# Kernel tuning notes

Hardware: AMD Instinct MI355X
Metric: run time of the kernel (lower is better)

## Reference

```python
import jax, jax.numpy as jnp
import numpy as np

PADDING_IDX = 0


def setup_inputs() -> dict:
    key = jax.random.key(0)
    k1, k2 = jax.random.split(key)
    B, S, D = 64, 2048, 128
    V = 200000
    grad_output = jax.random.normal(k1, (B, S, D), dtype=jnp.float32)
    indices = jax.random.randint(k2, (B, S), 0, V, dtype=jnp.int64)
    return {"grad_output": grad_output, "indices": indices, "num_embeddings": V}


def reference(grad_output, indices, num_embeddings):
    D = grad_output.shape[-1]
    flat_idx = indices.reshape(-1)                      # [B*S]
    flat_grad = grad_output.reshape(-1, D)              # [B*S, D]
    # Zero out contributions from padding positions; padding row stays 0,
    # matching the original (it never accumulates into padding_idx).
    mask = (flat_idx != PADDING_IDX)[:, None]           # [B*S, 1]
    masked_grad = jnp.where(mask, flat_grad, jnp.zeros((), dtype=flat_grad.dtype))
    dense_grad = jax.ops.segment_sum(masked_grad, flat_idx,
                                     num_segments=num_embeddings)
    return dense_grad.astype(jnp.float32)
```

## Files before the change

### kernel.cpp

```cpp
#include <hip/hip_runtime.h>


#define EMB_D   128
#define PAD_IDX 0
#define MAXC    8
#define OVF_CAP 16384

typedef float fvec4 __attribute__((ext_vector_type(4)));

__global__ void __launch_bounds__(256)
prefetch_zero(const float4* __restrict__ grad, long g4n,
              uint4* __restrict__ zreg, long zn4,
              float* __restrict__ sink) {
    long tid    = (long)blockIdx.x * 256 + threadIdx.x;
    long stride = (long)gridDim.x * 256;
    uint4 z = make_uint4(0u, 0u, 0u, 0u);
    for (long i = tid; i < zn4; i += stride) zreg[i] = z;
    float acc = 0.f;
    for (long i = tid; i < g4n; i += stride) {
        float4 g = grad[i];
        acc += g.x + g.y + g.z + g.w;
    }
    if (acc == 1234567.891f) sink[0] = acc;
}

__global__ void __launch_bounds__(256)
scatter_slots(const int* __restrict__ idx, unsigned* __restrict__ counts,
              unsigned* __restrict__ slots, unsigned* __restrict__ ovfcnt,
              uint2* __restrict__ ovf, int n) {
    int i = blockIdx.x * blockDim.x + threadIdx.x;
    if (i >= n) return;
    int e = idx[i];
    if (e == PAD_IDX) return;
    unsigned p = atomicAdd(&counts[e], 1u);
    if (p < MAXC) {
        slots[(size_t)e * MAXC + p] = (unsigned)i;
    } else {
        unsigned q = atomicAdd(ovfcnt, 1u);
        if (q < OVF_CAP) ovf[q] = make_uint2((unsigned)e, (unsigned)i);
    }
}

__global__ void __launch_bounds__(256)
reduce_write(const float* __restrict__ grad, const unsigned* __restrict__ counts,
             const uint4* __restrict__ slots4, const unsigned* __restrict__ ovfcnt,
             const uint2* __restrict__ ovf, float* __restrict__ out, int V) {
    int wid  = (blockIdx.x * 256 + (int)threadIdx.x) >> 6;
    int half = (threadIdx.x >> 5) & 1;
    int lane = threadIdx.x & 31;
    const float4* __restrict__ g4 = (const float4*)grad;

    int base = wid * 8;
    if (base >= V) return;

    int      vr[4];
    unsigned cs[4];
    uint4    s0[4];
    #pragma unroll
    for (int p = 0; p < 4; ++p) {
        int v = base + 2 * p + half;
        int vc = v < V ? v : V - 1;
        vr[p] = v;
        cs[p] = counts[vc];
        s0[p] = slots4[(size_t)vc * 2];
    }

    unsigned ia[4][4];
    float    msk[4][3];
    #pragma unroll
    for (int p = 0; p < 4; ++p) {
        unsigned c = cs[p];
        if (vr[p] >= V || vr[p] == PAD_IDX) c = 0u;
        cs[p] = c;
        uint4 s = s0[p];
        unsigned i0 = (c > 0u) ? s.x : 0u;
        ia[p][0] = i0;
        ia[p][1] = (c > 1u) ? s.y : i0;
        ia[p][2] = (c > 2u) ? s.z : i0;
        ia[p][3] = (c > 3u) ? s.w : i0;
        msk[p][0] = (c > 1u) ? 1.f : 0.f;
        msk[p][1] = (c > 2u) ? 1.f : 0.f;
        msk[p][2] = (c > 3u) ? 1.f : 0.f;
    }
    float4 g[4][4];
    #pragma unroll
    for (int p = 0; p < 4; ++p)
        #pragma unroll
        for (int k = 0; k < 4; ++k)
            g[p][k] = g4[(size_t)ia[p][k] * 32 + lane];

    float4 acc[4];
    #pragma unroll
    for (int p = 0; p < 4; ++p) {
        float z  = (cs[p] > 0u) ? 1.f : 0.f;
        float m1 = msk[p][0], m2 = msk[p][1], m3 = msk[p][2];
        acc[p].x = z * g[p][0].x + m1 * g[p][1].x + m2 * g[p][2].x + m3 * g[p][3].x;
        acc[p].y = z * g[p][0].y + m1 * g[p][1].y + m2 * g[p][2].y + m3 * g[p][3].y;
        acc[p].z = z * g[p][0].z + m1 * g[p][1].z + m2 * g[p][2].z + m3 * g[p][3].z;
        acc[p].w = z * g[p][0].w + m1 * g[p][1].w + m2 * g[p][2].w + m3 * g[p][3].w;
    }

    #pragma unroll
    for (int p = 0; p < 4; ++p) {
        unsigned c = cs[p];
        if (c > 4u) {
            int v = vr[p];
            uint4 s1 = slots4[(size_t)v * 2 + 1];
            unsigned j1 = (c > 5u) ? s1.y : s1.x;
            unsigned j2 = (c > 6u) ? s1.z : s1.x;
            unsigned j3 = (c > 7u) ? s1.w : s1.x;
            float4 b0 = g4[(size_t)s1.x * 32 + lane];
            float4 b1 = g4[(size_t)j1   * 32 + lane];
            float4 b2 = g4[(size_t)j2   * 32 + lane];
            float4 b3 = g4[(size_t)j3   * 32 + lane];
            float n1 = (c > 5u) ? 1.f : 0.f;
            float n2 = (c > 6u) ? 1.f : 0.f;
            float n3 = (c > 7u) ? 1.f : 0.f;
            acc[p].x += b0.x + n1 * b1.x + n2 * b2.x + n3 * b3.x;
            acc[p].y += b0.y + n1 * b1.y + n2 * b2.y + n3 * b3.y;
            acc[p].z += b0.z + n1 * b1.z + n2 * b2.z + n3 * b3.z;
            acc[p].w += b0.w + n1 * b1.w + n2 * b2.w + n3 * b3.w;
            if (c > (unsigned)MAXC) {
                unsigned n = *ovfcnt;
                if (n > OVF_CAP) n = OVF_CAP;
                for (unsigned q = 0; q < n; ++q) {
                    uint2 eo = ovf[q];
                    if (eo.x == (unsigned)v) {
                        float4 gg = g4[(size_t)eo.y * 32 + lane];
                        acc[p].x += gg.x; acc[p].y += gg.y;
                        acc[p].z += gg.z; acc[p].w += gg.w;
                    }
                }
            }
        }
    }

    #pragma unroll
    for (int p = 0; p < 4; ++p) {
        if (vr[p] < V) {
            fvec4 av = { acc[p].x, acc[p].y, acc[p].z, acc[p].w };
            __builtin_nontemporal_store(av, &((fvec4*)out)[(size_t)vr[p] * 32 + lane]);
        }
    }
}

__global__ void zero_f32x4(float4* __restrict__ p, long n4) {
    long i = (long)blockIdx.x * blockDim.x + threadIdx.x;
    long stride = (long)gridDim.x * blockDim.x;
    const float4 z = make_float4(0.f, 0.f, 0.f, 0.f);
    for (; i < n4; i += stride) p[i] = z;
}

__global__ void __launch_bounds__(256)
scatter_add_kernel(const float* __restrict__ grad, const int* __restrict__ idx,
                   float* __restrict__ out, int ntok) {
    int gid = blockIdx.x * blockDim.x + threadIdx.x;
    int token = gid >> 5;
    int d4 = gid & 31;
    if (token >= ntok) return;
    int e = idx[token];
    if (e == PAD_IDX) return;
    const float4 g = ((const float4*)grad)[(size_t)token * 32 + d4];
    float* dst = out + (size_t)e * EMB_D + d4 * 4;
    unsafeAtomicAdd(dst + 0, g.x);
    unsafeAtomicAdd(dst + 1, g.y);
    unsafeAtomicAdd(dst + 2, g.z);
    unsafeAtomicAdd(dst + 3, g.w);
}

extern "C" void kernel_launch(void* const* d_in, const int* in_sizes, int n_in,
                              void* d_out, int out_size, void* d_ws, size_t ws_size,
                              hipStream_t stream) {
    const float* grad = (const float*)d_in[0];
    const int*   idx  = (const int*)d_in[1];
    float*       out  = (float*)d_out;
    const int ntok = in_sizes[1];
    const int V = out_size / EMB_D;

    size_t off_counts = 0;
    size_t off_ovfcnt = off_counts + (size_t)V * 4;
    size_t off_slots  = off_ovfcnt + 16;
    size_t off_ovf    = off_slots + (size_t)V * MAXC * 4;
    size_t need       = off_ovf + (size_t)OVF_CAP * 8;

    if (ws_size < need) {
        zero_f32x4<<<4096, 256, 0, stream>>>((float4*)out, (long)out_size / 4);
        const int threads = ntok * 32;
        scatter_add_kernel<<<(threads + 255) / 256, 256, 0, stream>>>(grad, idx, out, ntok);
        return;
    }

    char* ws = (char*)d_ws;
    unsigned* counts = (unsigned*)(ws + off_counts);
    unsigned* ovfcnt = (unsigned*)(ws + off_ovfcnt);
    unsigned* slots  = (unsigned*)(ws + off_slots);
    uint2*    ovf    = (uint2*)(ws + off_ovf);

    {
        long zn4 = (long)(off_ovf - off_counts) / 16;
        long g4n = (long)ntok * (EMB_D / 4);
        float* sink = (float*)(ws + off_ovf);
        prefetch_zero<<<1024, 256, 0, stream>>>(
            (const float4*)grad, g4n, (uint4*)ws, zn4, sink);
    }

    scatter_slots<<<(ntok + 255) / 256, 256, 0, stream>>>(
        idx, counts, slots, ovfcnt, ovf, ntok);

    int waves   = (V + 7) / 8;
    int nblocks = (waves + 3) / 4;
    reduce_write<<<nblocks, 256, 0, stream>>>(
        grad, counts, (const uint4*)slots, ovfcnt, ovf, out, V);
}
```

Measured before the change: 173.7 us.

## Skip slot and gather loads for empty rows and stop zeroing the slot array

The reduce kernel now reads slot indices and gradient rows only when a row's count says they hold valid entries, where before it loaded all four gathers unconditionally and masked them with multiplies. Because slots are read only when backed by a count, the prefetch kernel now zeroes just the counts and overflow counter instead of the whole slot array. This cuts workspace memset traffic and wasted gathers. In exchange it adds branch divergence and serialises the dependent loads behind the count check. A dead duplicate assignment to zn4 remains.

Result: slower. 178.9 us (+3.0%).

```diff
diff --git a/kernel.cpp b/kernel.cpp
--- a/kernel.cpp
+++ b/kernel.cpp
@@ -53,73 +53,73 @@
     int base = wid * 8;
     if (base >= V) return;
 
-    int      vr[4];
     unsigned cs[4];
-    uint4    s0[4];
     #pragma unroll
     for (int p = 0; p < 4; ++p) {
         int v = base + 2 * p + half;
-        int vc = v < V ? v : V - 1;
-        vr[p] = v;
-        cs[p] = counts[vc];
-        s0[p] = slots4[(size_t)vc * 2];
-    }
-
-    unsigned ia[4][4];
-    float    msk[4][3];
-    #pragma unroll
-    for (int p = 0; p < 4; ++p) {
-        unsigned c = cs[p];
-        if (vr[p] >= V || vr[p] == PAD_IDX) c = 0u;
+        unsigned c = 0u;
+        if (v < V && v != PAD_IDX) c = counts[v];
         cs[p] = c;
-        uint4 s = s0[p];
-        unsigned i0 = (c > 0u) ? s.x : 0u;
-        ia[p][0] = i0;
-        ia[p][1] = (c > 1u) ? s.y : i0;
-        ia[p][2] = (c > 2u) ? s.z : i0;
-        ia[p][3] = (c > 3u) ? s.w : i0;
-        msk[p][0] = (c > 1u) ? 1.f : 0.f;
-        msk[p][1] = (c > 2u) ? 1.f : 0.f;
-        msk[p][2] = (c > 3u) ? 1.f : 0.f;
-    }
-    float4 g[4][4];
-    #pragma unroll
-    for (int p = 0; p < 4; ++p)
-        #pragma unroll
-        for (int k = 0; k < 4; ++k)
-            g[p][k] = g4[(size_t)ia[p][k] * 32 + lane];
+    }
+
+    uint4 s[4];
+    #pragma unroll
+    for (int p = 0; p < 4; ++p) {
+        s[p] = make_uint4(0u, 0u, 0u, 0u);
+        if (cs[p] > 0u) s[p] = slots4[(size_t)(base + 2 * p + half) * 2];
+    }
 
     float4 acc[4];
     #pragma unroll
-    for (int p = 0; p < 4; ++p) {
-        float z  = (cs[p] > 0u) ? 1.f : 0.f;
-        float m1 = msk[p][0], m2 = msk[p][1], m3 = msk[p][2];
-        acc[p].x = z * g[p][0].x + m1 * g[p][1].x + m2 * g[p][2].x + m3 * g[p][3].x;
-        acc[p].y = z * g[p][0].y + m1 * g[p][1].y + m2 * g[p][2].y + m3 * g[p][3].y;
-        acc[p].z = z * g[p][0].z + m1 * g[p][1].z + m2 * g[p][2].z + m3 * g[p][3].z;
-        acc[p].w = z * g[p][0].w + m1 * g[p][1].w + m2 * g[p][2].w + m3 * g[p][3].w;
-    }
+    for (int p = 0; p < 4; ++p) acc[p] = make_float4(0.f, 0.f, 0.f, 0.f);
+
+    #pragma unroll
+    for (int p = 0; p < 4; ++p)
+        if (cs[p] > 0u) {
+            float4 t = g4[(size_t)s[p].x * 32 + lane];
+            acc[p].x = t.x; acc[p].y = t.y; acc[p].z = t.z; acc[p].w = t.w;
+        }
+    #pragma unroll
+    for (int p = 0; p < 4; ++p)
+        if (cs[p] > 1u) {
+            float4 t = g4[(size_t)s[p].y * 32 + lane];
+            acc[p].x += t.x; acc[p].y += t.y; acc[p].z += t.z; acc[p].w += t.w;
+        }
+    #pragma unroll
+    for (int p = 0; p < 4; ++p)
+        if (cs[p] > 2u) {
+            float4 t = g4[(size_t)s[p].z * 32 + lane];
+            acc[p].x += t.x; acc[p].y += t.y; acc[p].z += t.z; acc[p].w += t.w;
+        }
+    #pragma unroll
+    for (int p = 0; p < 4; ++p)
+        if (cs[p] > 3u) {
+            float4 t = g4[(size_t)s[p].w * 32 + lane];
+            acc[p].x += t.x; acc[p].y += t.y; acc[p].z += t.z; acc[p].w += t.w;
+        }
 
     #pragma unroll
     for (int p = 0; p < 4; ++p) {
         unsigned c = cs[p];
         if (c > 4u) {
-            int v = vr[p];
+            int v = base + 2 * p + half;
             uint4 s1 = slots4[(size_t)v * 2 + 1];
-            unsigned j1 = (c > 5u) ? s1.y : s1.x;
-            unsigned j2 = (c > 6u) ? s1.z : s1.x;
-            unsigned j3 = (c > 7u) ? s1.w : s1.x;
-            float4 b0 = g4[(size_t)s1.x * 32 + lane];
-            float4 b1 = g4[(size_t)j1   * 32 + lane];
-            float4 b2 = g4[(size_t)j2   * 32 + lane];
-            float4 b3 = g4[(size_t)j3   * 32 + lane];
-            float n1 = (c > 5u) ? 1.f : 0.f;
-            float n2 = (c > 6u) ? 1.f : 0.f;
-            float n3 = (c > 7u) ? 1.f : 0.f;
-            acc[p].x += b0.x + n1 * b1.x + n2 * b2.x + n3 * b3.x;
-            acc[p].y += b0.y + n1 * b1.y + n2 * b2.y + n3 * b3.y;
-            acc[p].z += b0.z + n1 * b1.z + n2 * b2.z + n3 * b3.z;
-            acc[p].w += b0.w + n1 * b1.w + n2 * b2.w + n3 * b3.w;
+            {
+                float4 t = g4[(size_t)s1.x * 32 + lane];
+                acc[p].x += t.x; acc[p].y += t.y; acc[p].z += t.z; acc[p].w += t.w;
+            }
+            if (c > 5u) {
+                float4 t = g4[(size_t)s1.y * 32 + lane];
+                acc[p].x += t.x; acc[p].y += t.y; acc[p].z += t.z; acc[p].w += t.w;
+            }
+            if (c > 6u) {
+                float4 t = g4[(size_t)s1.z * 32 + lane];
+                acc[p].x += t.x; acc[p].y += t.y; acc[p].z += t.z; acc[p].w += t.w;
+            }
+            if (c > 7u) {
+                float4 t = g4[(size_t)s1.w * 32 + lane];
+                acc[p].x += t.x; acc[p].y += t.y; acc[p].z += t.z; acc[p].w += t.w;
+            }
             if (c > (unsigned)MAXC) {
                 unsigned n = *ovfcnt;
                 if (n > OVF_CAP) n = OVF_CAP;
@@ -137,9 +137,10 @@
 
     #pragma unroll
     for (int p = 0; p < 4; ++p) {
-        if (vr[p] < V) {
+        int v = base + 2 * p + half;
+        if (v < V) {
             fvec4 av = { acc[p].x, acc[p].y, acc[p].z, acc[p].w };
-            __builtin_nontemporal_store(av, &((fvec4*)out)[(size_t)vr[p] * 32 + lane]);
+            __builtin_nontemporal_store(av, &((fvec4*)out)[(size_t)v * 32 + lane]);
         }
     }
 }
@@ -197,7 +198,8 @@
     uint2*    ovf    = (uint2*)(ws + off_ovf);
 
     {
-        long zn4 = (long)(off_ovf - off_counts) / 16;
+        long zn4 = (long)(off_slots + 16 - off_counts) / 16;
+        zn4 = (long)off_slots / 16;
         long g4n = (long)ntok * (EMB_D / 4);
         float* sink = (float*)(ws + off_ovf);
         prefetch_zero<<<1024, 256, 0, stream>>>(
```
